# Performance work log

Measured on AMD Instinct MI355X. Metric: run time of the kernel, lower is better.

Reference implementation:

```python
import jax, jax.numpy as jnp
import numpy as np

LEAK = 0.95
NUM_STEPS = 10
THR = 1.0  # all layers get threshold = 1.0 in __init__

@jax.custom_vjp
def spike(x):
    # Surrogate_BP_Function.forward: heaviside(x > 0)
    return (x > 0).astype(x.dtype)

def _spike_fwd(x):
    return spike(x), x

def _spike_bwd(x, g):
    # backward: grad * 0.3 * relu(1 - |x|)
    return (g * 0.3 * jnp.maximum(1.0 - jnp.abs(x), 0.0),)

spike.defvjp(_spike_fwd, _spike_bwd)

def conv3x3(x, w):
    # stride 1, padding 1, no bias, NCHW / OIHW
    return jax.lax.conv_general_dilated(
        x, w, window_strides=(1, 1), padding=[(1, 1), (1, 1)],
        dimension_numbers=('NCHW', 'OIHW', 'NCHW'))

def avgpool2(x):
    b, c, h, w = x.shape
    return x.reshape(b, c, h // 2, 2, w // 2, 2).mean(axis=(3, 5))

def setup_inputs() -> dict:
    key = jax.random.key(0)
    ks = jax.random.split(key, 11)
    def w(k, shape, scale):
        return jax.random.normal(k, shape, dtype=jnp.float32) * scale
    inp = jax.random.normal(ks[0], (128, 3, 32, 32), dtype=jnp.float32)
    return {
        'inp': inp,
        'w1': w(ks[1], (64, 3, 3, 3), 0.35),
        'w2': w(ks[2], (64, 64, 3, 3), 0.1),
        'w3': w(ks[3], (128, 64, 3, 3), 0.1),
        'w4': w(ks[4], (128, 128, 3, 3), 0.08),
        'w5': w(ks[5], (256, 128, 3, 3), 0.08),
        'w6': w(ks[6], (256, 256, 3, 3), 0.06),
        'w7': w(ks[7], (256, 256, 3, 3), 0.06),
        'fc1_w': w(ks[8], (1024, 4096), 0.03),   # Linear(4*4*256, 1024)
        'fc2_w': w(ks[9], (10, 1024), 0.05),     # Linear(1024, 10)
    }

def reference(inp, w1, w2, w3, w4, w5, w6, w7, fc1_w, fc2_w):
    batch = inp.shape[0]
    conv_ws = [w2, w3, w4, w5, w6, w7]          # layers i = 1..6
    pool_after = [True, False, True, False, False, True]  # pool1 after i=1, pool2 after i=3, pool3 after i=6
    static = conv3x3(inp, w1)                   # static_input = conv1(inp)

    def step(carry, _):
        mem0, mem_fc1, mem_fc2 = carry
        # LIF update for conv1 (leaky accumulation of static input)
        mem0 = (1.0 - LEAK) * mem0 + LEAK * static
        thr = mem0 / THR - 1.0
        out_prev = spike(thr)
        mem0 = mem0 - jnp.where(thr > 0, THR, 0.0)  # soft reset
        # conv layers 2..7: membrane is OVERWRITTEN by the conv output each step
        for j, w in enumerate(conv_ws):
            m = conv3x3(out_prev, w)
            thr = m / THR - 1.0
            out_prev = spike(thr)
            if pool_after[j]:
                out_prev = avgpool2(out_prev)
        flat = out_prev.reshape(batch, -1)      # [B, 256*4*4]
        mem_fc1 = (1.0 - LEAK) * mem_fc1 + LEAK * (flat @ fc1_w.T)
        thr = mem_fc1 / THR - 1.0
        out = spike(thr)
        mem_fc1 = mem_fc1 - jnp.where(thr > 0, THR, 0.0)
        mem_fc2 = mem_fc2 + out @ fc2_w.T
        return (mem0, mem_fc1, mem_fc2), None

    init = (jnp.zeros_like(static),
            jnp.zeros((batch, 1024), dtype=inp.dtype),
            jnp.zeros((batch, fc2_w.shape[0]), dtype=inp.dtype))
    (mem0, mem_fc1, mem_fc2), _ = jax.lax.scan(step, init, None, length=NUM_STEPS)
    return mem_fc2 / NUM_STEPS
```

## Files before the change

kernel.cpp:

```cpp
#include <hip/hip_runtime.h>


typedef __attribute__((ext_vector_type(4))) int int32x4;

__device__ __forceinline__ float bf2f(ushort h) {
    union { unsigned u; float f; } v; v.u = ((unsigned)h) << 16;
    return v.f;
}
constexpr int ilog2(int x) { int r = 0; while (x > 1) { x >>= 1; ++r; } return r; }

__device__ __forceinline__ void gl_lds16(const void* g, void* l) {
    __builtin_amdgcn_global_load_lds(
        (const __attribute__((address_space(1))) unsigned int*)g,
        (__attribute__((address_space(3))) unsigned int*)l, 16, 0, 0);
}

#define SC21 4.76837158203125e-07
#define SC23 1.1920928955078125e-07

template <int IC, int OC>
__global__ void prep_convw_i8_k(const float* __restrict__ w, char* __restrict__ dst) {
    int idx = blockIdx.x * 256 + threadIdx.x;
    if (idx >= OC * IC * 9) return;
    int oc = idx / (IC * 9);
    int rem = idx % (IC * 9);
    int ic = rem / 9, q = rem % 9;
    int wq_ = (int)rintf(w[idx] * 2097152.0f);
    int a2 = ((wq_ + 128) & 255) - 128;
    int t2 = (wq_ - a2) >> 8;
    int a1 = ((t2 + 128) & 255) - 128;
    int a0 = (t2 - a1) >> 8;
    int sg = ic >> 6, kin = ic & 63, c = kin >> 4, bb = kin & 15;
    int oct = oc >> 6, ocl = oc & 63;
    constexpr int OCT = OC / 64;
    size_t base = ((size_t)(sg * 9 + q) * OCT + oct) * 12288;
    char digs[3] = {(char)a0, (char)a1, (char)a2};
#pragma unroll
    for (int s = 0; s < 3; ++s)
        dst[base + (size_t)(c * 192 + s * 64 + ocl) * 16 + bb] = digs[s];
}

__global__ void prep_fc1w_i8_k(const float* __restrict__ w, char* __restrict__ dst) {
    int idx = blockIdx.x * 256 + threadIdx.x;
    if (idx >= 1024 * 4096) return;
    int j = idx >> 12, k = idx & 4095;
    int c = k >> 4, hw = k & 15;
    int kp = hw * 256 + c;
    int wq_ = (int)rintf(w[idx] * 2097152.0f);
    int a2 = ((wq_ + 128) & 255) - 128;
    int t2 = (wq_ - a2) >> 8;
    int a1 = ((t2 + 128) & 255) - 128;
    int a0 = (t2 - a1) >> 8;
    int slab = kp >> 6, kin = kp & 63, cch = kin >> 4, bb = kin & 15;
    int oct = j >> 6, ocl = j & 63;
    size_t base = ((size_t)(slab * 16 + oct)) * 12288;
    char digs[3] = {(char)a0, (char)a1, (char)a2};
#pragma unroll
    for (int s = 0; s < 3; ++s)
        dst[base + (size_t)(cch * 192 + s * 64 + ocl) * 16 + bb] = digs[s];
}

template <int H, int C>
__global__ void halo0_k(char* __restrict__ buf) {
    constexpr int P = 4 * H + 4;
    constexpr int CPI = P * (C / 16);
    int idx = blockIdx.x * 256 + threadIdx.x;
    if (idx >= 1280 * CPI) return;
    int n = idx / CPI, r = idx % CPI;
    int p = r / (C / 16), c16 = r % (C / 16);
    int row, col;
    if (p < 2 * (H + 2)) { row = (p < H + 2) ? 0 : H + 1; col = p % (H + 2); }
    else { int qq = p - 2 * (H + 2); col = (qq < H) ? 0 : H + 1; row = 1 + (qq % H); }
    *(uint4*)&buf[(((size_t)n * (H + 2) + row) * (H + 2) + col) * C + c16 * 16] =
        (uint4){0u, 0u, 0u, 0u};
}

__global__ __launch_bounds__(256) void conv1lif_k(const float* __restrict__ inp,
                                                  const float* __restrict__ w1,
                                                  char* __restrict__ act1) {
    __shared__ float ws[27 * 64];
    for (int e = threadIdx.x; e < 1728; e += 256) {
        int oc = e / 27, j = e % 27;
        ws[j * 64 + oc] = w1[e];
    }
    __syncthreads();
    int t = blockIdx.x * 256 + threadIdx.x;
    int q = t & 3;
    int m = t >> 2;
    int n = m >> 10, h = (m >> 5) & 31, w = m & 31;
    float xv[27];
#pragma unroll
    for (int ic = 0; ic < 3; ++ic)
#pragma unroll
        for (int kh = 0; kh < 3; ++kh)
#pragma unroll
            for (int kw = 0; kw < 3; ++kw) {
                int r = h + kh - 1, c = w + kw - 1;
                xv[ic * 9 + kh * 3 + kw] =
                    (r >= 0 && r < 32 && c >= 0 && c < 32)
                        ? inp[(n * 3 + ic) * 1024 + r * 32 + c] : 0.0f;
            }
    float s[16], mem[16];
#pragma unroll
    for (int o = 0; o < 16; ++o) { s[o] = 0.f; mem[o] = 0.f; }
#pragma unroll
    for (int j = 0; j < 27; ++j) {
        float x = xv[j];
        const float* wr = &ws[j * 64 + q * 16];
#pragma unroll
        for (int o = 0; o < 16; ++o) s[o] += wr[o] * x;
    }
    const size_t dbase = (((size_t)h + 1) * 34 + (w + 1)) * 64 + q * 16;
    for (int st = 0; st < 10; ++st) {
        unsigned r[4];
#pragma unroll
        for (int g = 0; g < 4; ++g) {
            unsigned acc = 0;
#pragma unroll
            for (int e = 0; e < 4; ++e) {
                int o = g * 4 + e;
                mem[o] = 0.05f * mem[o] + 0.95f * s[o];
                unsigned b = (mem[o] > 1.f) ? 1u : 0u;
                mem[o] -= (float)b;
                acc |= b << (8 * e);
            }
            r[g] = acc;
        }
        size_t d = ((size_t)(st * 128 + n) * 34 * 34) * 64 + dbase;
        *(uint4*)&act1[d] = (uint4){r[0], r[1], r[2], r[3]};
    }
}

template <int H, int W, int IC, int OC, int NI, int MR, int EPI>
__global__ __launch_bounds__(256) void convi8_k(const char* __restrict__ act,
                                                const char* __restrict__ wq,
                                                char* __restrict__ outs,
                                                float scale) {
    constexpr int PW = W + 2, PHR = MR + 2;
    constexpr int MBLK = NI * MR * W;
    constexpr int NPIX = NI * PHR * PW;
    constexpr int ACH = NPIX * 4;
    constexpr int HR = (ACH + 255) / 256;
    constexpr int SLABS = IC / 64;
    constexpr int OCT = OC / 64;
    constexpr int LHW = ilog2(H * W), LW2 = ilog2(W), LMW = ilog2(MR * W);
    static_assert(MBLK == 128, "tile mapping");

    __shared__ __align__(16) char sA[NPIX * 64];

    const int tid = threadIdx.x, lane = tid & 63;
    const int wid = tid >> 6, wm = wid >> 1, wn = wid & 1;
    const int b = blockIdx.x, oct = blockIdx.y;
    const int oc0 = oct * 64;
    const int m0 = b * MBLK;
    constexpr int TPI = (NI == 1) ? (H / MR) : 1;
    const int n0 = (NI == 1) ? (b / TPI) : (b * NI);
    const int h0 = (NI == 1) ? (b % TPI) * MR : 0;

    int asrc[HR]; bool apred[HR];
#pragma unroll
    for (int r = 0; r < HR; ++r) {
        int i = r * 256 + tid;
        apred[r] = (i < ACH);
        int ii = apred[r] ? i : 0;
        int c = ii / NPIX, pix = ii % NPIX;
        int pc = pix % PW, t2 = pix / PW;
        int hp = t2 % PHR, img = t2 / PHR;
        asrc[r] = (((n0 + img) * (H + 2) + h0 + hp) * PW + pc) * IC + c * 16;
    }
    int apix[4];
#pragma unroll
    for (int am = 0; am < 4; ++am) {
        int p = wm * 64 + am * 16 + (lane & 15);
        int img = p >> LMW;
        int pi = p & ((MR * W) - 1);
        int h = pi >> LW2;
        apix[am] = (img * PHR + h) * PW + (pi & (W - 1));
    }
    const int cA = lane >> 4;
    const int lan15 = lane & 15;

    int32x4 acc[3][4][2];
#pragma unroll
    for (int s = 0; s < 3; ++s)
#pragma unroll
        for (int a = 0; a < 4; ++a)
#pragma unroll
            for (int bn = 0; bn < 2; ++bn) acc[s][a][bn] = (int32x4){0, 0, 0, 0};

    constexpr size_t USTRIDE = (size_t)OCT * 12288;
    const char* wqlane = wq + (size_t)oct * 12288
                       + (size_t)(cA * 192 + wn * 32 + lan15) * 16;

    auto stage_A = [&](int sl_) {
#pragma unroll
        for (int r = 0; r < HR; ++r)
            if (apred[r]) gl_lds16(act + asrc[r] + sl_ * 64, sA + (r * 256 + tid) * 16);
    };

    stage_A(0);
    asm volatile("s_waitcnt vmcnt(0)" ::: "memory");
    __builtin_amdgcn_s_barrier();

    for (int sl = 0; sl < SLABS; ++sl) {
        const char* wslab = wqlane + (size_t)sl * 9 * USTRIDE;
#pragma unroll
        for (int t = 0; t < 9; ++t) {
            const char* wt = wslab + (size_t)t * USTRIDE;
            int32x4 bf[3][2];
#pragma unroll
            for (int s = 0; s < 3; ++s)
#pragma unroll
                for (int bn = 0; bn < 2; ++bn)
                    bf[s][bn] = *(const int32x4*)(wt + s * 1024 + bn * 256);
            const int qr = t / 3, qc = t - qr * 3;
            int32x4 af[4];
#pragma unroll
            for (int am = 0; am < 4; ++am)
                af[am] = *(const int32x4*)&sA[(cA * NPIX + apix[am] + qr * PW + qc) * 16];
            __builtin_amdgcn_s_setprio(1);
#pragma unroll
            for (int s = 0; s < 3; ++s)
#pragma unroll
                for (int bn = 0; bn < 2; ++bn)
#pragma unroll
                    for (int am = 0; am < 4; ++am)
                        acc[s][am][bn] = __builtin_amdgcn_mfma_i32_16x16x64_i8(
                            af[am], bf[s][bn], acc[s][am][bn], 0, 0, 0);
            __builtin_amdgcn_s_setprio(0);
        }
        if (sl + 1 < SLABS) {
            asm volatile("s_waitcnt lgkmcnt(0)" ::: "memory");
            __builtin_amdgcn_s_barrier();
            stage_A(sl + 1);
            asm volatile("s_waitcnt vmcnt(0)" ::: "memory");
            __builtin_amdgcn_s_barrier();
        }
    }

#pragma unroll
    for (int am = 0; am < 4; ++am)
#pragma unroll
        for (int bn = 0; bn < 2; ++bn)
#pragma unroll
            for (int rr = 0; rr < 4; ++rr) {
                int rl = wm * 64 + am * 16 + (lane >> 4) * 4 + rr;
                int col = oc0 + wn * 32 + bn * 16 + (lane & 15);
                int m = m0 + rl;
                float v = (float)((65536.0 * (double)acc[0][am][bn][rr]
                                 + 256.0 * (double)acc[1][am][bn][rr]
                                 + (double)acc[2][am][bn][rr]) * (double)scale);
                char sp = (v > 1.0f) ? (char)1 : (char)0;
                if (EPI == 1) {
                    int n = m >> LHW, h = (m >> LW2) & (H - 1), w = m & (W - 1);
                    outs[((size_t)(n * (H + 2) + h + 1) * PW + (w + 1)) * OC + col] = sp;
                } else {
                    outs[(size_t)m * OC + col] = sp;
                }
            }
}

template <int C, int HI>
__global__ void pool_i8_k(const char* __restrict__ in, char* __restrict__ out) {
    constexpr int HO = HI / 2, C16 = C / 16;
    constexpr int TOT = 1280 * HO * HO * C16;
    int idx = blockIdx.x * 256 + threadIdx.x;
    if (idx >= TOT) return;
    int c16 = idx % C16;
    int t = idx / C16;
    int w = t % HO; t /= HO;
    int h = t % HO;
    int n = t / HO;
    const char* p = in + ((size_t)(n * HI + 2 * h) * HI + 2 * w) * C + c16 * 16;
    uint4 a0 = *(const uint4*)p;
    uint4 a1 = *(const uint4*)(p + C);
    uint4 a2 = *(const uint4*)(p + (size_t)HI * C);
    uint4 a3 = *(const uint4*)(p + (size_t)HI * C + C);
    uint4 r;
    r.x = a0.x + a1.x + a2.x + a3.x;
    r.y = a0.y + a1.y + a2.y + a3.y;
    r.z = a0.z + a1.z + a2.z + a3.z;
    r.w = a0.w + a1.w + a2.w + a3.w;
    *(uint4*)&out[((size_t)(n * (HO + 2) + h + 1) * (HO + 2) + (w + 1)) * C + c16 * 16] = r;
}

__global__ void pool3q_k(const char* __restrict__ in, char* __restrict__ out) {
    int idx = blockIdx.x * 256 + threadIdx.x;
    if (idx >= 327680) return;
    int c16 = idx & 15;
    int t = idx >> 4;
    int wo = t & 3, ho = (t >> 2) & 3, n = t >> 4;
    const char* p = in + ((size_t)(n * 8 + 2 * ho) * 8 + 2 * wo) * 256 + c16 * 16;
    uint4 a0 = *(const uint4*)p;
    uint4 a1 = *(const uint4*)(p + 256);
    uint4 a2 = *(const uint4*)(p + 2048);
    uint4 a3 = *(const uint4*)(p + 2048 + 256);
    uint4 r;
    r.x = a0.x + a1.x + a2.x + a3.x;
    r.y = a0.y + a1.y + a2.y + a3.y;
    r.z = a0.z + a1.z + a2.z + a3.z;
    r.w = a0.w + a1.w + a2.w + a3.w;
    *(uint4*)&out[((size_t)(n * 16 + ho * 4 + wo) * 16 + c16) * 16] = r;
}

__global__ __launch_bounds__(256) void fc1i8_k(const char* __restrict__ A,
                                               const char* __restrict__ wq,
                                               float* __restrict__ part) {
    __shared__ __align__(16) char sA[2][8192];
    __shared__ __align__(16) char sB[2][12288];
    const int tid = threadIdx.x, lane = tid & 63;
    const int wid = tid >> 6, wm = wid >> 1, wn = wid & 1;
    const int m0 = blockIdx.x * 128, oct = blockIdx.y, kt = blockIdx.z;

    int32x4 acc[3][4][2];
#pragma unroll
    for (int s = 0; s < 3; ++s)
#pragma unroll
        for (int a = 0; a < 4; ++a)
#pragma unroll
            for (int bn = 0; bn < 2; ++bn) acc[s][a][bn] = (int32x4){0, 0, 0, 0};

    auto stageA = [&](int sg, int bf_) {
#pragma unroll
        for (int r = 0; r < 2; ++r) {
            int i = r * 256 + tid;
            int c = i >> 7, pix = i & 127;
            gl_lds16(A + (size_t)(m0 + pix) * 4096 + sg * 64 + c * 16,
                     sA[bf_] + (size_t)i * 16);
        }
    };
    auto stageB = [&](int sg, int bf_) {
        const char* src = wq + ((size_t)(sg * 16 + oct)) * 12288 + tid * 16;
#pragma unroll
        for (int r = 0; r < 3; ++r)
            gl_lds16(src + r * 4096, sB[bf_] + (r * 256 + tid) * 16);
    };

    int buf = 0;
    stageA(kt * 32, 0);
    stageB(kt * 32, 0);
    __syncthreads();
    const int cA = lane >> 4;
    for (int sl = 0; sl < 32; ++sl) {
        int sg = kt * 32 + sl;
        if (sl < 31) { stageA(sg + 1, buf ^ 1); stageB(sg + 1, buf ^ 1); }
        int32x4 af[4];
#pragma unroll
        for (int am = 0; am < 4; ++am)
            af[am] = *(const int32x4*)&sA[buf][(cA * 128 + wm * 64 + am * 16 + (lane & 15)) * 16];
#pragma unroll
        for (int s = 0; s < 3; ++s)
#pragma unroll
            for (int bn = 0; bn < 2; ++bn) {
                int R = s * 64 + wn * 32 + bn * 16 + (lane & 15);
                int32x4 bf = *(const int32x4*)&sB[buf][(cA * 192 + R) * 16];
#pragma unroll
                for (int am = 0; am < 4; ++am)
                    acc[s][am][bn] = __builtin_amdgcn_mfma_i32_16x16x64_i8(
                        af[am], bf, acc[s][am][bn], 0, 0, 0);
            }
        if (sl < 31) { __syncthreads(); buf ^= 1; }
    }
#pragma unroll
    for (int am = 0; am < 4; ++am)
#pragma unroll
        for (int bn = 0; bn < 2; ++bn)
#pragma unroll
            for (int rr = 0; rr < 4; ++rr) {
                int row = m0 + wm * 64 + am * 16 + (lane >> 4) * 4 + rr;
                int col = oct * 64 + wn * 32 + bn * 16 + (lane & 15);
                float v = (float)((65536.0 * (double)acc[0][am][bn][rr]
                                 + 256.0 * (double)acc[1][am][bn][rr]
                                 + (double)acc[2][am][bn][rr]) * SC23);
                part[((size_t)kt * 1280 + row) * 1024 + col] = v;
            }
}

__global__ void fc1lif_k(const float* __restrict__ part, ushort* __restrict__ sbuf) {
    int idx = blockIdx.x * 256 + threadIdx.x;
    int n = idx >> 10, j = idx & 1023;
    float m = 0.f;
    for (int t = 0; t < 10; ++t) {
        size_t row = (size_t)(t * 128 + n) * 1024 + j;
        float y = part[row] + part[1310720 + row];
        m = 0.05f * m + 0.95f * y;
        float sp = (m > 1.f) ? 1.f : 0.f;
        m -= sp;
        sbuf[row] = sp > 0.f ? (ushort)0x3F80 : (ushort)0;
    }
}

__global__ __launch_bounds__(256) void fc2o_k(const ushort* __restrict__ S,
                                              const float* __restrict__ W2,
                                              float* __restrict__ out) {
    __shared__ float wsh[10 * 1024];
    __shared__ float red[10][256];
    int n = blockIdx.x, tid = threadIdx.x;
    for (int e = tid; e < 10240; e += 256) wsh[e] = W2[e];
    __syncthreads();
    float accv = 0.f;
    for (int t = 0; t < 10; ++t) {
        const ushort* sp = S + ((size_t)(t * 128 + n)) * 1024 + tid * 4;
        float s0 = bf2f(sp[0]), s1 = bf2f(sp[1]), s2 = bf2f(sp[2]), s3 = bf2f(sp[3]);
#pragma unroll
        for (int o = 0; o < 10; ++o) {
            const float* w = &wsh[o * 1024 + tid * 4];
            red[o][tid] = s0 * w[0] + s1 * w[1] + s2 * w[2] + s3 * w[3];
        }
        __syncthreads();
        for (int off = 128; off >= 1; off >>= 1) {
            if (tid < off) {
#pragma unroll
                for (int o = 0; o < 10; ++o) red[o][tid] += red[o][tid + off];
            }
            __syncthreads();
        }
        if (tid < 10) accv += red[tid][0];
        __syncthreads();
    }
    if (tid < 10) out[n * 10 + tid] = accv * 0.1f;
}

extern "C" void kernel_launch(void* const* d_in, const int* in_sizes, int n_in,
                              void* d_out, int out_size, void* d_ws, size_t ws_size,
                              hipStream_t stream) {
    const float* inp  = (const float*)d_in[0];
    const float* w1   = (const float*)d_in[1];
    const float* w2   = (const float*)d_in[2];
    const float* w3   = (const float*)d_in[3];
    const float* w4   = (const float*)d_in[4];
    const float* w5   = (const float*)d_in[5];
    const float* w6   = (const float*)d_in[6];
    const float* w7   = (const float*)d_in[7];
    const float* fc1w = (const float*)d_in[8];
    const float* fc2w = (const float*)d_in[9];
    float* out = (float*)d_out;

    char* base = (char*)d_ws;
    char* arenaA = base;
    char* arenaB = base + 94679040;
    size_t o = 94679040 + 83886080;
    auto alloc = [&](size_t bytes) { void* p = base + o; o += (bytes + 255) & ~(size_t)255; return p; };
    char*   wq2  = (char*)alloc(110592);
    char*   wq3  = (char*)alloc(221184);
    char*   wq4  = (char*)alloc(442368);
    char*   wq5  = (char*)alloc(884736);
    char*   wq6  = (char*)alloc(1769472);
    char*   wq7  = (char*)alloc(1769472);
    char*   wqf1 = (char*)alloc(12582912);
    ushort* sbuf = (ushort*)alloc(2621440);
    (void)ws_size;

    char*  act1  = arenaA;
    char*  c2out = arenaB;
    char*  act2  = arenaA;
    char*  c3out = arenaB;
    char*  c4out = arenaA;
    char*  act3  = arenaA + 41943040;
    char*  c5out = arenaB;
    char*  c6out = arenaB + 33554432;
    char*  c7out = arenaA;
    char*  afc1  = arenaA + 20971520;
    float* part  = (float*)(arenaA + 26214400);

    prep_convw_i8_k<64, 64>  <<<(36864 + 255) / 256, 256, 0, stream>>>(w2, wq2);
    prep_convw_i8_k<64, 128> <<<(73728 + 255) / 256, 256, 0, stream>>>(w3, wq3);
    prep_convw_i8_k<128, 128><<<(147456 + 255) / 256, 256, 0, stream>>>(w4, wq4);
    prep_convw_i8_k<128, 256><<<(294912 + 255) / 256, 256, 0, stream>>>(w5, wq5);
    prep_convw_i8_k<256, 256><<<(589824 + 255) / 256, 256, 0, stream>>>(w6, wq6);
    prep_convw_i8_k<256, 256><<<(589824 + 255) / 256, 256, 0, stream>>>(w7, wq7);
    prep_fc1w_i8_k<<<(4194304 + 255) / 256, 256, 0, stream>>>(fc1w, wqf1);

    halo0_k<32, 64><<<(1280 * 132 * 4 + 255) / 256, 256, 0, stream>>>(act1);
    conv1lif_k<<<2048, 256, 0, stream>>>(inp, w1, act1);

    convi8_k<32, 32, 64, 64, 1, 4, 0>
        <<<dim3(10240, 1), 256, 0, stream>>>(act1, wq2, c2out, (float)SC21);
    halo0_k<16, 64><<<(1280 * 68 * 4 + 255) / 256, 256, 0, stream>>>(act2);
    pool_i8_k<64, 32><<<(1280 * 256 * 4 + 255) / 256, 256, 0, stream>>>(c2out, act2);

    halo0_k<16, 128><<<(1280 * 68 * 8 + 255) / 256, 256, 0, stream>>>(c3out);
    convi8_k<16, 16, 64, 128, 1, 8, 1>
        <<<dim3(2560, 2), 256, 0, stream>>>(act2, wq3, c3out, (float)SC23);
    convi8_k<16, 16, 128, 128, 1, 8, 0>
        <<<dim3(2560, 2), 256, 0, stream>>>(c3out, wq4, c4out, (float)SC21);
    halo0_k<8, 128><<<(1280 * 36 * 8 + 255) / 256, 256, 0, stream>>>(act3);
    pool_i8_k<128, 16><<<(1280 * 64 * 8 + 255) / 256, 256, 0, stream>>>(c4out, act3);

    halo0_k<8, 256><<<(1280 * 36 * 16 + 255) / 256, 256, 0, stream>>>(c5out);
    convi8_k<8, 8, 128, 256, 2, 8, 1>
        <<<dim3(640, 4), 256, 0, stream>>>(act3, wq5, c5out, (float)SC23);
    halo0_k<8, 256><<<(1280 * 36 * 16 + 255) / 256, 256, 0, stream>>>(c6out);
    convi8_k<8, 8, 256, 256, 2, 8, 1>
        <<<dim3(640, 4), 256, 0, stream>>>(c5out, wq6, c6out, (float)SC21);
    convi8_k<8, 8, 256, 256, 2, 8, 0>
        <<<dim3(640, 4), 256, 0, stream>>>(c6out, wq7, c7out, (float)SC21);

    pool3q_k<<<(327680 + 255) / 256, 256, 0, stream>>>(c7out, afc1);

    fc1i8_k<<<dim3(10, 16, 2), 256, 0, stream>>>(afc1, wqf1, part);
    fc1lif_k<<<512, 256, 0, stream>>>(part, sbuf);
    fc2o_k<<<128, 256, 0, stream>>>(sbuf, fc2w, out);
}
```

Measured before the change: 916.9 us.

## Double the conv tile to 512 threads and stage weights through LDS

The int8 conv kernel now runs with 512 threads, so each block covers 256 output pixels instead of 128. Weight fragments are no longer read by each wave straight from global memory. Instead they are loaded asynchronously into a double-buffered LDS tile per filter tap and shared across waves. The goal is to cut redundant global weight traffic and amortize activation staging over more pixels. In exchange it adds a block-wide barrier on every tap, needs more LDS per block, and halves the grid size, which may lower occupancy and overlap.

New measurement: 987.2 us. +7.7%, slower.

```diff
diff --git a/kernel.cpp b/kernel.cpp
--- a/kernel.cpp
+++ b/kernel.cpp
@@ -132,7 +132,7 @@
 }
 
 template <int H, int W, int IC, int OC, int NI, int MR, int EPI>
-__global__ __launch_bounds__(256) void convi8_k(const char* __restrict__ act,
+__global__ __launch_bounds__(512) void convi8_k(const char* __restrict__ act,
                                                 const char* __restrict__ wq,
                                                 char* __restrict__ outs,
                                                 float scale) {
@@ -140,16 +140,19 @@
     constexpr int MBLK = NI * MR * W;
     constexpr int NPIX = NI * PHR * PW;
     constexpr int ACH = NPIX * 4;
-    constexpr int HR = (ACH + 255) / 256;
+    constexpr int HR = (ACH + 511) / 512;
     constexpr int SLABS = IC / 64;
     constexpr int OCT = OC / 64;
+    constexpr int U = SLABS * 9;
     constexpr int LHW = ilog2(H * W), LW2 = ilog2(W), LMW = ilog2(MR * W);
-    static_assert(MBLK == 128, "tile mapping");
+    static_assert(MBLK == 256, "tile mapping");
 
     __shared__ __align__(16) char sA[NPIX * 64];
+    __shared__ __align__(16) char sB[2][12288];
 
     const int tid = threadIdx.x, lane = tid & 63;
-    const int wid = tid >> 6, wm = wid >> 1, wn = wid & 1;
+    const int wid = tid >> 6;
+    const int wm = wid >> 1, wn = wid & 1;
     const int b = blockIdx.x, oct = blockIdx.y;
     const int oc0 = oct * 64;
     const int m0 = b * MBLK;
@@ -160,7 +163,7 @@
     int asrc[HR]; bool apred[HR];
 #pragma unroll
     for (int r = 0; r < HR; ++r) {
-        int i = r * 256 + tid;
+        int i = r * 512 + tid;
         apred[r] = (i < ACH);
         int ii = apred[r] ? i : 0;
         int c = ii / NPIX, pix = ii % NPIX;
@@ -188,32 +191,31 @@
 #pragma unroll
             for (int bn = 0; bn < 2; ++bn) acc[s][a][bn] = (int32x4){0, 0, 0, 0};
 
-    constexpr size_t USTRIDE = (size_t)OCT * 12288;
-    const char* wqlane = wq + (size_t)oct * 12288
-                       + (size_t)(cA * 192 + wn * 32 + lan15) * 16;
-
+    const size_t wqoct = (size_t)oct * 12288;
+
+    auto stage_B = [&](int unit, int bufc) {
+        const char* wsrc = wq + (size_t)unit * (OCT * 12288) + wqoct;
+        gl_lds16(wsrc + tid * 16, sB[bufc] + tid * 16);
+        if (tid < 256)
+            gl_lds16(wsrc + 8192 + tid * 16, sB[bufc] + 8192 + tid * 16);
+    };
     auto stage_A = [&](int sl_) {
 #pragma unroll
         for (int r = 0; r < HR; ++r)
-            if (apred[r]) gl_lds16(act + asrc[r] + sl_ * 64, sA + (r * 256 + tid) * 16);
+            if (apred[r]) gl_lds16(act + asrc[r] + sl_ * 64, sA + (r * 512 + tid) * 16);
     };
 
     stage_A(0);
-    asm volatile("s_waitcnt vmcnt(0)" ::: "memory");
-    __builtin_amdgcn_s_barrier();
-
+    stage_B(0, 0);
+    __syncthreads();
+
+    int buf = 0;
     for (int sl = 0; sl < SLABS; ++sl) {
-        const char* wslab = wqlane + (size_t)sl * 9 * USTRIDE;
-#pragma unroll
-        for (int t = 0; t < 9; ++t) {
-            const char* wt = wslab + (size_t)t * USTRIDE;
-            int32x4 bf[3][2];
-#pragma unroll
-            for (int s = 0; s < 3; ++s)
-#pragma unroll
-                for (int bn = 0; bn < 2; ++bn)
-                    bf[s][bn] = *(const int32x4*)(wt + s * 1024 + bn * 256);
-            const int qr = t / 3, qc = t - qr * 3;
+#pragma unroll
+        for (int q = 0; q < 9; ++q) {
+            const int u = sl * 9 + q;
+            if (u + 1 < U) stage_B(u + 1, buf ^ 1);
+            const int qr = q / 3, qc = q - qr * 3;
             int32x4 af[4];
 #pragma unroll
             for (int am = 0; am < 4; ++am)
@@ -222,19 +224,21 @@
 #pragma unroll
             for (int s = 0; s < 3; ++s)
 #pragma unroll
-                for (int bn = 0; bn < 2; ++bn)
+                for (int bn = 0; bn < 2; ++bn) {
+                    int R = s * 64 + wn * 32 + bn * 16 + lan15;
+                    int32x4 bf = *(const int32x4*)&sB[buf][(cA * 192 + R) * 16];
 #pragma unroll
                     for (int am = 0; am < 4; ++am)
                         acc[s][am][bn] = __builtin_amdgcn_mfma_i32_16x16x64_i8(
-                            af[am], bf[s][bn], acc[s][am][bn], 0, 0, 0);
+                            af[am], bf, acc[s][am][bn], 0, 0, 0);
+                }
             __builtin_amdgcn_s_setprio(0);
+            __syncthreads();
+            buf ^= 1;
         }
         if (sl + 1 < SLABS) {
-            asm volatile("s_waitcnt lgkmcnt(0)" ::: "memory");
-            __builtin_amdgcn_s_barrier();
             stage_A(sl + 1);
-            asm volatile("s_waitcnt vmcnt(0)" ::: "memory");
-            __builtin_amdgcn_s_barrier();
+            __syncthreads();
         }
     }
 
@@ -474,27 +478,27 @@
     halo0_k<32, 64><<<(1280 * 132 * 4 + 255) / 256, 256, 0, stream>>>(act1);
     conv1lif_k<<<2048, 256, 0, stream>>>(inp, w1, act1);
 
-    convi8_k<32, 32, 64, 64, 1, 4, 0>
-        <<<dim3(10240, 1), 256, 0, stream>>>(act1, wq2, c2out, (float)SC21);
+    convi8_k<32, 32, 64, 64, 1, 8, 0>
+        <<<dim3(5120, 1), 512, 0, stream>>>(act1, wq2, c2out, (float)SC21);
     halo0_k<16, 64><<<(1280 * 68 * 4 + 255) / 256, 256, 0, stream>>>(act2);
     pool_i8_k<64, 32><<<(1280 * 256 * 4 + 255) / 256, 256, 0, stream>>>(c2out, act2);
 
     halo0_k<16, 128><<<(1280 * 68 * 8 + 255) / 256, 256, 0, stream>>>(c3out);
-    convi8_k<16, 16, 64, 128, 1, 8, 1>
-        <<<dim3(2560, 2), 256, 0, stream>>>(act2, wq3, c3out, (float)SC23);
-    convi8_k<16, 16, 128, 128, 1, 8, 0>
-        <<<dim3(2560, 2), 256, 0, stream>>>(c3out, wq4, c4out, (float)SC21);
+    convi8_k<16, 16, 64, 128, 1, 16, 1>
+        <<<dim3(1280, 2), 512, 0, stream>>>(act2, wq3, c3out, (float)SC23);
+    convi8_k<16, 16, 128, 128, 1, 16, 0>
+        <<<dim3(1280, 2), 512, 0, stream>>>(c3out, wq4, c4out, (float)SC21);
     halo0_k<8, 128><<<(1280 * 36 * 8 + 255) / 256, 256, 0, stream>>>(act3);
     pool_i8_k<128, 16><<<(1280 * 64 * 8 + 255) / 256, 256, 0, stream>>>(c4out, act3);
 
     halo0_k<8, 256><<<(1280 * 36 * 16 + 255) / 256, 256, 0, stream>>>(c5out);
-    convi8_k<8, 8, 128, 256, 2, 8, 1>
-        <<<dim3(640, 4), 256, 0, stream>>>(act3, wq5, c5out, (float)SC23);
+    convi8_k<8, 8, 128, 256, 4, 8, 1>
+        <<<dim3(320, 4), 512, 0, stream>>>(act3, wq5, c5out, (float)SC23);
     halo0_k<8, 256><<<(1280 * 36 * 16 + 255) / 256, 256, 0, stream>>>(c6out);
-    convi8_k<8, 8, 256, 256, 2, 8, 1>
-        <<<dim3(640, 4), 256, 0, stream>>>(c5out, wq6, c6out, (float)SC21);
-    convi8_k<8, 8, 256, 256, 2, 8, 0>
-        <<<dim3(640, 4), 256, 0, stream>>>(c6out, wq7, c7out, (float)SC21);
+    convi8_k<8, 8, 256, 256, 4, 8, 1>
+        <<<dim3(320, 4), 512, 0, stream>>>(c5out, wq6, c6out, (float)SC21);
+    convi8_k<8, 8, 256, 256, 4, 8, 0>
+        <<<dim3(320, 4), 512, 0, stream>>>(c6out, wq7, c7out, (float)SC21);
 
     pool3q_k<<<(327680 + 255) / 256, 256, 0, stream>>>(c7out, afc1);
 
```
